# Kernel optimization log

Hardware: AMD Instinct MI355X
Metric: run time of the kernel (lower is better)

## Reference

```python
import jax, jax.numpy as jnp
import numpy as np

ALPHA = 1.0

def setup_inputs() -> dict:
    key = jax.random.key(0)
    k1, k2 = jax.random.split(key)
    N, K, D = 524288, 256, 256
    context = jax.random.normal(k1, (N, D), dtype=jnp.float32)
    clusters = jax.random.normal(k2, (K, D), dtype=jnp.float32)
    return {"context": context, "clusters": clusters}

def reference(context, clusters):
    # Squared euclidean distance via the matmul trick: same math as
    # sum((x[:,None]-c)**2, -1) but avoids materializing (N,K,D).
    x2 = jnp.sum(context * context, axis=1, keepdims=True)          # (N,1)
    c2 = jnp.sum(clusters * clusters, axis=1)                       # (K,)
    xc = context @ clusters.T                                       # (N,K)
    distance = x2 + c2 - 2.0 * xc                                   # (N,K)
    q = 1.0 / (1.0 + distance / ALPHA)
    q = q ** ((ALPHA + 1.0) / 2.0)
    q = q / jnp.sum(q, axis=1, keepdims=True)                        # row-normalize
    return q
```

## Files before the change

kernel.cpp:

```cpp
#include <hip/hip_runtime.h>
#include <hip/hip_bf16.h>


#define DD 256
#define KC 256
#define BM 32
#define CL_SHORTS (KC * DD)

typedef __attribute__((ext_vector_type(4)))  float f32x4;
typedef __attribute__((ext_vector_type(16))) float f32x16;
typedef __attribute__((ext_vector_type(8)))  short bf16x8;
typedef __attribute__((ext_vector_type(4)))  short bf16x4;

__device__ __forceinline__ short f2bf(float f) {
    union { float f; unsigned u; } v; v.f = f;
    unsigned r = (v.u + 0x7fffu + ((v.u >> 16) & 1u)) >> 16;
    return (short)r;
}

__device__ __forceinline__ f32x4 ld4(const float* p) { return *(const f32x4*)p; }

__global__ __launch_bounds__(64)
void prep_clusters(const float* __restrict__ clus,
                   short* __restrict__ wsb, float* __restrict__ c2) {
    const int c = blockIdx.x;
    const int t = threadIdx.x;
    f32x4 v = *(const f32x4*)(clus + c * DD + t * 4);
    bf16x4 o;
    o[0] = f2bf(v[0]); o[1] = f2bf(v[1]); o[2] = f2bf(v[2]); o[3] = f2bf(v[3]);

    const int j    = t >> 1;
    const int ks   = j >> 1;
    const int hi   = j & 1;
    const int half = t & 1;
    const int nj   = c >> 5;
    const int l31  = c & 31;
    *(bf16x4*)&wsb[(((nj * 16 + ks) * 64 + hi * 32 + l31) << 3) + half * 4] = o;

    float s = v[0]*v[0] + v[1]*v[1] + v[2]*v[2] + v[3]*v[3];
    s += __shfl_xor(s, 1);  s += __shfl_xor(s, 2);  s += __shfl_xor(s, 4);
    s += __shfl_xor(s, 8);  s += __shfl_xor(s, 16); s += __shfl_xor(s, 32);
    if (t == 0) c2[c] = s;
}

__global__ __launch_bounds__(256, 5)
void cluster_q_main(const float* __restrict__ ctx,
                    const short* __restrict__ wsb,
                    const float* __restrict__ c2g,
                    float* __restrict__ out) {
    __shared__ short Af[32 * 32 * 8];
    __shared__ float x2p4[4][BM];
    __shared__ float rowsum[4][BM];

    const int t    = threadIdx.x;
    const int lane = t & 63;
    const int w    = t >> 6;
    const int l31  = lane & 31;
    const int hi   = lane >> 5;
    const size_t row0 = (size_t)blockIdx.x * BM;

    {
        const int r    = lane >> 1;
        const int half = lane & 1;
        const float* src = ctx + (row0 + (size_t)r) * DD + w * 64 + half * 32;
        f32x4 u[8];
#pragma unroll
        for (int i = 0; i < 4; ++i) {
            u[2*i]   = ld4(src + i * 8);
            u[2*i+1] = ld4(src + i * 8 + 4);
        }
        float xs = 0.f;
#pragma unroll
        for (int i = 0; i < 4; ++i) {
            f32x4 a0 = u[2*i], a1 = u[2*i+1];
            bf16x8 o;
            o[0] = f2bf(a0[0]); o[1] = f2bf(a0[1]);
            o[2] = f2bf(a0[2]); o[3] = f2bf(a0[3]);
            o[4] = f2bf(a1[0]); o[5] = f2bf(a1[1]);
            o[6] = f2bf(a1[2]); o[7] = f2bf(a1[3]);
            xs += a0[0]*a0[0] + a0[1]*a0[1] + a0[2]*a0[2] + a0[3]*a0[3]
                + a1[0]*a1[0] + a1[1]*a1[1] + a1[2]*a1[2] + a1[3]*a1[3];
            const int j = w * 8 + half * 4 + i;
            *(bf16x8*)&Af[(j * 32 + r) * 8] = o;
        }
        xs += __shfl_xor(xs, 1);
        if (half == 0) x2p4[w][r] = xs;
    }

    const short* bl = wsb + (size_t)(w * 2 * 16) * 512 + lane * 8;

    __syncthreads();

    const float x2l = x2p4[0][l31] + x2p4[1][l31] + x2p4[2][l31] + x2p4[3][l31];

    f32x16 acc[2];
    acc[0] = (f32x16)0.f;
    acc[1] = (f32x16)0.f;

    bf16x8 bs[3][2];
#pragma unroll
    for (int p = 0; p < 2; ++p)
#pragma unroll
        for (int j2 = 0; j2 < 2; ++j2)
            bs[p][j2] = *(const bf16x8*)(bl + (j2 * 16 + p) * 512);

    bf16x8 afA = *(const bf16x8*)&Af[((0 * 2 + hi) * 32 + l31) * 8];
    bf16x8 afB;

#pragma unroll
    for (int ks = 0; ks < 16; ++ks) {
        const bool even = (ks & 1) == 0;
        const int cur   = ks % 3;
        const int nxt   = (ks + 2) % 3;

        if (ks < 14) {
#pragma unroll
            for (int j2 = 0; j2 < 2; ++j2)
                bs[nxt][j2] = *(const bf16x8*)(bl + (j2 * 16 + ks + 2) * 512);
        }
        if (ks < 15) {
            bf16x8 v = *(const bf16x8*)&Af[(((ks + 1) * 2 + hi) * 32 + l31) * 8];
            if (even) afB = v; else afA = v;
        }

        const bf16x8 af = even ? afA : afB;
#pragma unroll
        for (int j2 = 0; j2 < 2; ++j2)
            acc[j2] = __builtin_amdgcn_mfma_f32_32x32x16_bf16(
                af, bs[cur][j2], acc[j2], 0, 0, 0);
    }

    float c2v[2];
#pragma unroll
    for (int j2 = 0; j2 < 2; ++j2) c2v[j2] = c2g[w * 64 + j2 * 32 + l31];

#pragma unroll
    for (int r = 0; r < 16; ++r) {
        const int rr = (r & 3) + 8 * (r >> 2) + 4 * hi;
        const float x2r = __shfl(x2l, rr);
        float s = 0.f;
#pragma unroll
        for (int j2 = 0; j2 < 2; ++j2) {
            float d = x2r + c2v[j2] - 2.f * acc[j2][r];
            float q = 1.f / (1.f + d);
            acc[j2][r] = q;
            s += q;
        }
        s += __shfl_xor(s, 1);
        s += __shfl_xor(s, 2);
        s += __shfl_xor(s, 4);
        s += __shfl_xor(s, 8);
        s += __shfl_xor(s, 16);
        if (l31 == 0) rowsum[w][rr] = s;
    }
    __syncthreads();

#pragma unroll
    for (int r = 0; r < 16; ++r) {
        const int rr = (r & 3) + 8 * (r >> 2) + 4 * hi;
        const float inv = 1.f / (rowsum[0][rr] + rowsum[1][rr] +
                                 rowsum[2][rr] + rowsum[3][rr]);
        float* op = out + (row0 + (size_t)rr) * KC + w * 64 + l31;
#pragma unroll
        for (int j2 = 0; j2 < 2; ++j2)
            op[j2 * 32] = acc[j2][r] * inv;
    }
}

extern "C" void kernel_launch(void* const* d_in, const int* in_sizes, int n_in,
                              void* d_out, int out_size, void* d_ws, size_t ws_size,
                              hipStream_t stream) {
    const float* ctx  = (const float*)d_in[0];
    const float* clus = (const float*)d_in[1];
    float* out = (float*)d_out;

    short* wsb = (short*)d_ws;
    float* c2  = (float*)((char*)d_ws + CL_SHORTS * 2);

    const int nrows = in_sizes[0] / DD;
    const int grid  = nrows / BM;

    hipLaunchKernelGGL(prep_clusters, dim3(KC), dim3(64), 0, stream, clus, wsb, c2);
    hipLaunchKernelGGL(cluster_q_main, dim3(grid), dim3(256), 0, stream,
                       ctx, wsb, c2, out);
}
```

Baseline: 290.9 us.

## Process multiple row tiles per block with double-buffered context prefetch

Each block now loops over 8 row tiles instead of one. The next tile's context rows are loaded into registers during the current tile's MFMA and epilogue, then converted into a second LDS buffer. This is meant to hide global load latency and amortise per-block setup such as the c2 loads. In exchange, the launch-bounds occupancy hint drops from 5 to 3 and the grid becomes smaller.

```diff
diff --git a/kernel.cpp b/kernel.cpp
--- a/kernel.cpp
+++ b/kernel.cpp
@@ -5,6 +5,7 @@
 #define DD 256
 #define KC 256
 #define BM 32
+#define NT 8
 #define CL_SHORTS (KC * DD)
 
 typedef __attribute__((ext_vector_type(4)))  float f32x4;
@@ -43,13 +44,13 @@
     if (t == 0) c2[c] = s;
 }
 
-__global__ __launch_bounds__(256, 5)
+__global__ __launch_bounds__(256, 3)
 void cluster_q_main(const float* __restrict__ ctx,
                     const short* __restrict__ wsb,
                     const float* __restrict__ c2g,
                     float* __restrict__ out) {
-    __shared__ short Af[32 * 32 * 8];
-    __shared__ float x2p4[4][BM];
+    __shared__ short Af[2][32 * 32 * 8];
+    __shared__ float x2p4[2][4][BM];
     __shared__ float rowsum[4][BM];
 
     const int t    = threadIdx.x;
@@ -57,18 +58,26 @@
     const int w    = t >> 6;
     const int l31  = lane & 31;
     const int hi   = lane >> 5;
-    const size_t row0 = (size_t)blockIdx.x * BM;
-
+    const int r_st    = lane >> 1;
+    const int half_st = lane & 1;
+
+    const size_t row_blk = (size_t)blockIdx.x * (NT * BM);
+
+    const short* bl = wsb + (size_t)(w * 2 * 16) * 512 + lane * 8;
+    float c2v[2];
+    c2v[0] = c2g[w * 64 + l31];
+    c2v[1] = c2g[w * 64 + 32 + l31];
+
+    const float* srcbase = ctx + (row_blk + (size_t)r_st) * DD + w * 64 + half_st * 32;
+
+    f32x4 u[8];
+
+#pragma unroll
+    for (int i = 0; i < 4; ++i) {
+        u[2*i]   = ld4(srcbase + i * 8);
+        u[2*i+1] = ld4(srcbase + i * 8 + 4);
+    }
     {
-        const int r    = lane >> 1;
-        const int half = lane & 1;
-        const float* src = ctx + (row0 + (size_t)r) * DD + w * 64 + half * 32;
-        f32x4 u[8];
-#pragma unroll
-        for (int i = 0; i < 4; ++i) {
-            u[2*i]   = ld4(src + i * 8);
-            u[2*i+1] = ld4(src + i * 8 + 4);
-        }
         float xs = 0.f;
 #pragma unroll
         for (int i = 0; i < 4; ++i) {
@@ -80,90 +89,116 @@
             o[6] = f2bf(a1[2]); o[7] = f2bf(a1[3]);
             xs += a0[0]*a0[0] + a0[1]*a0[1] + a0[2]*a0[2] + a0[3]*a0[3]
                 + a1[0]*a1[0] + a1[1]*a1[1] + a1[2]*a1[2] + a1[3]*a1[3];
-            const int j = w * 8 + half * 4 + i;
-            *(bf16x8*)&Af[(j * 32 + r) * 8] = o;
+            const int j = w * 8 + half_st * 4 + i;
+            *(bf16x8*)&Af[0][(j * 32 + r_st) * 8] = o;
         }
         xs += __shfl_xor(xs, 1);
-        if (half == 0) x2p4[w][r] = xs;
-    }
-
-    const short* bl = wsb + (size_t)(w * 2 * 16) * 512 + lane * 8;
-
-    __syncthreads();
-
-    const float x2l = x2p4[0][l31] + x2p4[1][l31] + x2p4[2][l31] + x2p4[3][l31];
-
-    f32x16 acc[2];
-    acc[0] = (f32x16)0.f;
-    acc[1] = (f32x16)0.f;
-
-    bf16x8 bs[3][2];
-#pragma unroll
-    for (int p = 0; p < 2; ++p)
-#pragma unroll
-        for (int j2 = 0; j2 < 2; ++j2)
-            bs[p][j2] = *(const bf16x8*)(bl + (j2 * 16 + p) * 512);
-
-    bf16x8 afA = *(const bf16x8*)&Af[((0 * 2 + hi) * 32 + l31) * 8];
-    bf16x8 afB;
-
-#pragma unroll
-    for (int ks = 0; ks < 16; ++ks) {
-        const bool even = (ks & 1) == 0;
-        const int cur   = ks % 3;
-        const int nxt   = (ks + 2) % 3;
-
-        if (ks < 14) {
-#pragma unroll
-            for (int j2 = 0; j2 < 2; ++j2)
-                bs[nxt][j2] = *(const bf16x8*)(bl + (j2 * 16 + ks + 2) * 512);
-        }
-        if (ks < 15) {
-            bf16x8 v = *(const bf16x8*)&Af[(((ks + 1) * 2 + hi) * 32 + l31) * 8];
-            if (even) afB = v; else afA = v;
-        }
-
-        const bf16x8 af = even ? afA : afB;
-#pragma unroll
-        for (int j2 = 0; j2 < 2; ++j2)
-            acc[j2] = __builtin_amdgcn_mfma_f32_32x32x16_bf16(
-                af, bs[cur][j2], acc[j2], 0, 0, 0);
-    }
-
-    float c2v[2];
-#pragma unroll
-    for (int j2 = 0; j2 < 2; ++j2) c2v[j2] = c2g[w * 64 + j2 * 32 + l31];
-
-#pragma unroll
-    for (int r = 0; r < 16; ++r) {
-        const int rr = (r & 3) + 8 * (r >> 2) + 4 * hi;
-        const float x2r = __shfl(x2l, rr);
-        float s = 0.f;
-#pragma unroll
-        for (int j2 = 0; j2 < 2; ++j2) {
-            float d = x2r + c2v[j2] - 2.f * acc[j2][r];
-            float q = 1.f / (1.f + d);
-            acc[j2][r] = q;
-            s += q;
-        }
-        s += __shfl_xor(s, 1);
-        s += __shfl_xor(s, 2);
-        s += __shfl_xor(s, 4);
-        s += __shfl_xor(s, 8);
-        s += __shfl_xor(s, 16);
-        if (l31 == 0) rowsum[w][rr] = s;
+        if (half_st == 0) x2p4[0][w][r_st] = xs;
     }
     __syncthreads();
 
-#pragma unroll
-    for (int r = 0; r < 16; ++r) {
-        const int rr = (r & 3) + 8 * (r >> 2) + 4 * hi;
-        const float inv = 1.f / (rowsum[0][rr] + rowsum[1][rr] +
-                                 rowsum[2][rr] + rowsum[3][rr]);
-        float* op = out + (row0 + (size_t)rr) * KC + w * 64 + l31;
-#pragma unroll
-        for (int j2 = 0; j2 < 2; ++j2)
-            op[j2 * 32] = acc[j2][r] * inv;
+#pragma unroll 2
+    for (int it = 0; it < NT; ++it) {
+        const int cur = it & 1;
+        const int nxt = cur ^ 1;
+        const size_t trow = row_blk + (size_t)it * BM;
+
+        const float x2l = x2p4[cur][0][l31] + x2p4[cur][1][l31]
+                        + x2p4[cur][2][l31] + x2p4[cur][3][l31];
+
+        f32x16 acc[2];
+        acc[0] = (f32x16)0.f;
+        acc[1] = (f32x16)0.f;
+
+        const short* AfC = &Af[cur][0];
+
+        bf16x8 bs[3][2];
+#pragma unroll
+        for (int p = 0; p < 2; ++p)
+#pragma unroll
+            for (int j2 = 0; j2 < 2; ++j2)
+                bs[p][j2] = *(const bf16x8*)(bl + (j2 * 16 + p) * 512);
+
+        bf16x8 af[3];
+        af[0] = *(const bf16x8*)&AfC[((0 * 2 + hi) * 32 + l31) * 8];
+        af[1] = *(const bf16x8*)&AfC[((1 * 2 + hi) * 32 + l31) * 8];
+
+#pragma unroll
+        for (int ks = 0; ks < 16; ++ks) {
+            const int cA = ks % 3;
+            if (ks < 14) {
+                const int nx = (ks + 2) % 3;
+#pragma unroll
+                for (int j2 = 0; j2 < 2; ++j2)
+                    bs[nx][j2] = *(const bf16x8*)(bl + (j2 * 16 + ks + 2) * 512);
+                af[nx] = *(const bf16x8*)&AfC[(((ks + 2) * 2 + hi) * 32 + l31) * 8];
+            }
+#pragma unroll
+            for (int j2 = 0; j2 < 2; ++j2)
+                acc[j2] = __builtin_amdgcn_mfma_f32_32x32x16_bf16(
+                    af[cA], bs[cA][j2], acc[j2], 0, 0, 0);
+        }
+
+        if (it + 1 < NT) {
+            const float* s2 = srcbase + (size_t)(it + 1) * BM * DD;
+#pragma unroll
+            for (int i = 0; i < 4; ++i) {
+                u[2*i]   = ld4(s2 + i * 8);
+                u[2*i+1] = ld4(s2 + i * 8 + 4);
+            }
+        }
+
+#pragma unroll
+        for (int r = 0; r < 16; ++r) {
+            const int rr = (r & 3) + 8 * (r >> 2) + 4 * hi;
+            const float x2r = __shfl(x2l, rr);
+            float s = 0.f;
+#pragma unroll
+            for (int j2 = 0; j2 < 2; ++j2) {
+                float d = x2r + c2v[j2] - 2.f * acc[j2][r];
+                float q = 1.f / (1.f + d);
+                acc[j2][r] = q;
+                s += q;
+            }
+            s += __shfl_xor(s, 1);
+            s += __shfl_xor(s, 2);
+            s += __shfl_xor(s, 4);
+            s += __shfl_xor(s, 8);
+            s += __shfl_xor(s, 16);
+            if (l31 == 0) rowsum[w][rr] = s;
+        }
+        __syncthreads();
+
+#pragma unroll
+        for (int r = 0; r < 16; ++r) {
+            const int rr = (r & 3) + 8 * (r >> 2) + 4 * hi;
+            const float inv = 1.f / (rowsum[0][rr] + rowsum[1][rr] +
+                                     rowsum[2][rr] + rowsum[3][rr]);
+            float* op = out + (trow + (size_t)rr) * KC + w * 64 + l31;
+#pragma unroll
+            for (int j2 = 0; j2 < 2; ++j2)
+                op[j2 * 32] = acc[j2][r] * inv;
+        }
+
+        if (it + 1 < NT) {
+            float xs = 0.f;
+#pragma unroll
+            for (int i = 0; i < 4; ++i) {
+                f32x4 a0 = u[2*i], a1 = u[2*i+1];
+                bf16x8 o;
+                o[0] = f2bf(a0[0]); o[1] = f2bf(a0[1]);
+                o[2] = f2bf(a0[2]); o[3] = f2bf(a0[3]);
+                o[4] = f2bf(a1[0]); o[5] = f2bf(a1[1]);
+                o[6] = f2bf(a1[2]); o[7] = f2bf(a1[3]);
+                xs += a0[0]*a0[0] + a0[1]*a0[1] + a0[2]*a0[2] + a0[3]*a0[3]
+                    + a1[0]*a1[0] + a1[1]*a1[1] + a1[2]*a1[2] + a1[3]*a1[3];
+                const int j = w * 8 + half_st * 4 + i;
+                *(bf16x8*)&Af[nxt][(j * 32 + r_st) * 8] = o;
+            }
+            xs += __shfl_xor(xs, 1);
+            if (half_st == 0) x2p4[nxt][w][r_st] = xs;
+        }
+        __syncthreads();
     }
 }
 
@@ -178,7 +213,7 @@
     float* c2  = (float*)((char*)d_ws + CL_SHORTS * 2);
 
     const int nrows = in_sizes[0] / DD;
-    const int grid  = nrows / BM;
+    const int grid  = nrows / (BM * NT);
 
     hipLaunchKernelGGL(prep_clusters, dim3(KC), dim3(64), 0, stream, clus, wsb, c2);
     hipLaunchKernelGGL(cluster_q_main, dim3(grid), dim3(256), 0, stream,
```

After: 443.8 us. 1.53x slower.
